# Performance work log

Measured on AMD Instinct MI355X. Metric: run time of the kernel, lower is better.

The kernel has to match this reference:

```python
import jax, jax.numpy as jnp
import numpy as np

N = 100000
E = 1600000
IN_CH, HID_CH, OUT_CH = 128, 64, 32


def setup_inputs() -> dict:
    key = jax.random.key(0)
    ks = jax.random.split(key, 6)
    x = jax.random.normal(ks[0], (N, IN_CH), dtype=jnp.float32)
    ei = jax.random.randint(ks[1], (2, E), 0, N, dtype=jnp.int64)
    W1 = jax.random.normal(ks[2], (IN_CH, HID_CH), dtype=jnp.float32) * 0.05
    b1 = jax.random.normal(ks[3], (HID_CH,), dtype=jnp.float32) * 0.05
    W2 = jax.random.normal(ks[4], (HID_CH, OUT_CH), dtype=jnp.float32) * 0.05
    b2 = jax.random.normal(ks[5], (OUT_CH,), dtype=jnp.float32) * 0.05
    return {"x": x, "ei": ei, "W1": W1, "b1": b1, "W2": W2, "b2": b2}


def gcn_layer(x, sa, da, n):
    # degree with self-loops already appended in sa/da
    deg = jax.ops.segment_sum(jnp.ones((sa.shape[0],), x.dtype), da, num_segments=n)
    prod = deg[sa] * deg[da]
    norm = jnp.where(prod > 0, jax.lax.rsqrt(prod), 0.0)  # (deg_s*deg_d)^-0.5, inf->0
    msg = x[sa] * norm[:, None]            # [E+N, C] gather + scale
    return jax.ops.segment_sum(msg, da, num_segments=n)  # scatter_add


def reference(x, ei, W1, b1, W2, b2):
    n = x.shape[0]
    loop = jnp.arange(n, dtype=ei.dtype)
    sa = jnp.concatenate([ei[0], loop])
    da = jnp.concatenate([ei[1], loop])
    h = gcn_layer(x @ W1 + b1, sa, da, n)
    h = jax.nn.relu(h)
    # dropout: eval mode (training=False) -> identity
    return gcn_layer(h @ W2 + b2, sa, da, n)
```

## Files before the change

### kernel.cpp

```cpp
#include <hip/hip_runtime.h>

#define NN 100000
#define NE 1600000
#define IN_CH 128
#define HID_CH 64
#define OUT_CH 32
#define NB2 98
#define CHUNKA 8192
#define NBLKA ((NE + CHUNKA - 1) / CHUNKA)
#define NBLK_GEMM ((NN + 63) / 64)

typedef unsigned short ushort_t;
typedef _Float16 half2_t __attribute__((ext_vector_type(2)));
typedef float f32x2 __attribute__((ext_vector_type(2)));

__device__ inline ushort_t f2bf(float f) {
    union { float f; unsigned u; } v; v.f = f;
    unsigned r = v.u + 0x7fff + ((v.u >> 16) & 1);
    return (ushort_t)(r >> 16);
}
__device__ inline float blo(unsigned u) {
    union { unsigned x; float f; } v; v.x = u << 16; return v.f;
}
__device__ inline float bhi(unsigned u) {
    union { unsigned x; float f; } v; v.x = u & 0xffff0000u; return v.f;
}
__device__ inline unsigned pkh(float a, float b) {
    union { half2_t h; unsigned u; } v;
    v.h[0] = (_Float16)a; v.h[1] = (_Float16)b;
    return v.u;
}
__device__ inline half2_t u2h(unsigned u) {
    union { unsigned u; half2_t h; } v; v.u = u; return v.h;
}
__device__ inline float fdot2(unsigned a, unsigned b, float c) {
#if __has_builtin(__builtin_amdgcn_fdot2)
    return __builtin_amdgcn_fdot2(u2h(a), u2h(b), c, false);
#else
    half2_t ha = u2h(a), hb = u2h(b);
    return c + (float)ha[0] * (float)hb[0] + (float)ha[1] * (float)hb[1];
#endif
}
__device__ inline f32x2 pk_add(f32x2 a, f32x2 b) {
    f32x2 r;
    asm("v_pk_add_f32 %0, %1, %2" : "=v"(r) : "v"(a), "v"(b));
    return r;
}

__global__ __launch_bounds__(256) void k_bhist(const int* __restrict__ da,
                                               int* __restrict__ bcnt,
                                               int* __restrict__ bhall) {
    __shared__ int hist[4][NB2];
    int t = threadIdx.x, w = t >> 6;
    for (int i = t; i < 4 * NB2; i += 256) ((int*)hist)[i] = 0;
    __syncthreads();
    int base = blockIdx.x * CHUNKA;
    for (int i = 0; i < CHUNKA; i += 256) {
        int e = base + i + t;
        if (e < NE) atomicAdd(&hist[w][da[e] >> 10], 1);
    }
    __syncthreads();
    if (t < NB2) {
        int c = hist[0][t] + hist[1][t] + hist[2][t] + hist[3][t];
        bhall[blockIdx.x * NB2 + t] = c;
        if (c) atomicAdd(&bcnt[t], c);
    }
}

__global__ __launch_bounds__(128) void k_bscan(const int* __restrict__ bcnt,
                                               int* __restrict__ bbase,
                                               int* __restrict__ bcur,
                                               int* __restrict__ rowptr) {
    __shared__ int lds[128];
    int t = threadIdx.x;
    int v = (t < NB2) ? bcnt[t] : 0;
    lds[t] = v;
    __syncthreads();
    for (int off = 1; off < 128; off <<= 1) {
        int x = (t >= off) ? lds[t - off] : 0;
        __syncthreads();
        lds[t] += x;
        __syncthreads();
    }
    int excl = lds[t] - v;
    if (t < NB2) { bbase[t] = excl; bcur[t] = excl; }
    if (t == 0) { bbase[NB2] = NE; rowptr[NN] = NE; }
}

__global__ __launch_bounds__(256) void k_bfill(const int* __restrict__ sa,
                                               const int* __restrict__ da,
                                               const int* __restrict__ bhall,
                                               int* __restrict__ bcur,
                                               unsigned* __restrict__ ebuf) {
    __shared__ int lcur[NB2];
    int t = threadIdx.x;
    if (t < NB2) {
        int c = bhall[blockIdx.x * NB2 + t];
        lcur[t] = c ? atomicAdd(&bcur[t], c) : 0;
    }
    __syncthreads();
    int base = blockIdx.x * CHUNKA;
    for (int i = 0; i < CHUNKA; i += 256) {
        int e = base + i + t;
        if (e < NE) {
            int d = da[e];
            int p = atomicAdd(&lcur[d >> 10], 1);
            ebuf[p] = ((unsigned)sa[e] << 10) | (unsigned)(d & 1023);
        }
    }
}

__global__ __launch_bounds__(1024) void k_bfine(const unsigned* __restrict__ ebuf,
                                                const int* __restrict__ bbase,
                                                int* __restrict__ rowptr,
                                                float* __restrict__ rs,
                                                int* __restrict__ col) {
    __shared__ int cnt[1024];
    __shared__ int cur[1024];
    __shared__ int scn[1024];
    int b = blockIdx.x, t = threadIdx.x;
    int nb = NN - b * 1024; if (nb > 1024) nb = 1024;
    int beg = bbase[b], end = bbase[b + 1];
    cnt[t] = 0;
    __syncthreads();
    for (int i = beg + t; i < end; i += 1024) atomicAdd(&cnt[ebuf[i] & 1023], 1);
    __syncthreads();
    int v = cnt[t];
    scn[t] = v;
    __syncthreads();
    for (int off = 1; off < 1024; off <<= 1) {
        int x = (t >= off) ? scn[t - off] : 0;
        __syncthreads();
        scn[t] += x;
        __syncthreads();
    }
    int excl = scn[t] - v;
    if (t < nb) {
        rowptr[b * 1024 + t] = beg + excl;
        rs[b * 1024 + t] = rsqrtf((float)(v + 1));
        cur[t] = beg + excl;
    }
    __syncthreads();
    for (int i = beg + t; i < end; i += 1024) {
        unsigned p = ebuf[i];
        int pos = atomicAdd(&cur[p & 1023], 1);
        col[pos] = (int)(p >> 10);
    }
}

#define SWZU1(n, k2) ((n) * 64 + ((k2) ^ ((((n) & 7)) << 2)))
#define SWZ2(n, k) ((n) * 64 + ((k) ^ ((((n) & 7)) << 2)))

__global__ __launch_bounds__(256, 4) void k_gemm1(
    const float* __restrict__ x, const float* __restrict__ W1,
    const float* __restrict__ b1, const float* __restrict__ rs,
    ushort_t* __restrict__ xsb) {
    __shared__ unsigned xth[64 * 64];
    __shared__ unsigned w1h[64 * 64];
    int t = threadIdx.x;
    int base = blockIdx.x * 64;

#pragma unroll
    for (int i = 0; i < 8; ++i) {
        int flat = i * 1024 + t * 4;
        int node = flat >> 7, k0 = flat & 127;
        int gn = base + node;
        float4 v = make_float4(0.f, 0.f, 0.f, 0.f);
        if (gn < NN) v = *(const float4*)(x + (size_t)gn * IN_CH + k0);
        uint2 pk;
        pk.x = pkh(v.x, v.y);
        pk.y = pkh(v.z, v.w);
        *(uint2*)&xth[SWZU1(node, k0 >> 1)] = pk;
    }
#pragma unroll
    for (int i = 0; i < 16; ++i) {
        int idx = i * 256 + t;
        int k2 = idx >> 6, c = idx & 63;
        float f0 = W1[(2 * k2) * 64 + c];
        float f1 = W1[(2 * k2 + 1) * 64 + c];
        w1h[idx] = pkh(f0, f1);
    }
    __syncthreads();

    int tn = t & 15, tc = t >> 4;
    int c0 = tc * 4;
    float acc[4][4];
#pragma unroll
    for (int a = 0; a < 4; ++a)
#pragma unroll
        for (int b = 0; b < 4; ++b) acc[a][b] = 0.f;

    for (int k2 = 0; k2 < 64; k2 += 2) {
        uint2 xu[4];
#pragma unroll
        for (int jn = 0; jn < 4; ++jn)
            xu[jn] = *(uint2*)&xth[SWZU1(tn + jn * 16, k2)];
        uint4 w0 = *(uint4*)&w1h[(k2 + 0) * 64 + c0];
        uint4 w1 = *(uint4*)&w1h[(k2 + 1) * 64 + c0];
        unsigned wq0[4] = {w0.x, w0.y, w0.z, w0.w};
        unsigned wq1[4] = {w1.x, w1.y, w1.z, w1.w};
#pragma unroll
        for (int jn = 0; jn < 4; ++jn)
#pragma unroll
            for (int jc = 0; jc < 4; ++jc) {
                acc[jn][jc] = fdot2(xu[jn].x, wq0[jc], acc[jn][jc]);
                acc[jn][jc] = fdot2(xu[jn].y, wq1[jc], acc[jn][jc]);
            }
    }

    float4 bb = *(const float4*)&b1[c0];
#pragma unroll
    for (int jn = 0; jn < 4; ++jn) {
        int gn = base + tn + jn * 16;
        if (gn < NN) {
            float r = rs[gn];
            uint2 pk;
            pk.x = (unsigned)f2bf((acc[jn][0] + bb.x) * r) |
                   ((unsigned)f2bf((acc[jn][1] + bb.y) * r) << 16);
            pk.y = (unsigned)f2bf((acc[jn][2] + bb.z) * r) |
                   ((unsigned)f2bf((acc[jn][3] + bb.w) * r) << 16);
            *(uint2*)&xsb[(size_t)gn * HID_CH + c0] = pk;
        }
    }
}

#define ADD8PK(v) do { \
    f32x2 w0_, w1_, w2_, w3_; \
    w0_.x = blo((v).x); w0_.y = bhi((v).x); p0 = pk_add(p0, w0_); \
    w1_.x = blo((v).y); w1_.y = bhi((v).y); p1 = pk_add(p1, w1_); \
    w2_.x = blo((v).z); w2_.y = bhi((v).z); p2 = pk_add(p2, w2_); \
    w3_.x = blo((v).w); w3_.y = bhi((v).w); p3 = pk_add(p3, w3_); } while (0)

__global__ __launch_bounds__(256) void k_agg1(
    const int* __restrict__ rowptr, const int* __restrict__ col,
    const ushort_t* __restrict__ xsb, const float* __restrict__ rs,
    ushort_t* __restrict__ hb) {
    int gid = blockIdx.x * blockDim.x + threadIdx.x;
    int n = gid >> 6;
    if (n >= NN) return;
    int lane = threadIdx.x & 63;
    int g = lane >> 3;
    unsigned c0 = (unsigned)(lane & 7) * 8;
    int beg = rowptr[n], end = rowptr[n + 1];

    f32x2 p0 = {0.f, 0.f}, p1 = {0.f, 0.f}, p2 = {0.f, 0.f}, p3 = {0.f, 0.f};
    if (g == 0) {
        uint4 sv = *(const uint4*)&xsb[(unsigned)n * 64u + c0];
        ADD8PK(sv);
    }

    int i = beg;
    for (; i + 16 <= end; i += 16) {
        int s0 = col[i + g];
        int s1 = col[i + 8 + g];
        uint4 v0 = *(const uint4*)&xsb[(unsigned)s0 * 64u + c0];
        uint4 v1 = *(const uint4*)&xsb[(unsigned)s1 * 64u + c0];
        ADD8PK(v0);
        ADD8PK(v1);
    }
    if (i + 8 <= end) {
        int s0 = col[i + g];
        uint4 v0 = *(const uint4*)&xsb[(unsigned)s0 * 64u + c0];
        ADD8PK(v0);
        i += 8;
    }
    int r = end - i;
    if (g < r) {
        int s0 = col[i + g];
        uint4 v0 = *(const uint4*)&xsb[(unsigned)s0 * 64u + c0];
        ADD8PK(v0);
    }

    float a0 = p0.x, a1 = p0.y, a2 = p1.x, a3 = p1.y;
    float a4 = p2.x, a5 = p2.y, a6 = p3.x, a7 = p3.y;
#pragma unroll
    for (int m = 8; m <= 32; m <<= 1) {
        a0 += __shfl_xor(a0, m); a1 += __shfl_xor(a1, m);
        a2 += __shfl_xor(a2, m); a3 += __shfl_xor(a3, m);
        a4 += __shfl_xor(a4, m); a5 += __shfl_xor(a5, m);
        a6 += __shfl_xor(a6, m); a7 += __shfl_xor(a7, m);
    }

    if (g == 0) {
        float rn = rs[n];
        uint4 pk;
        pk.x = (unsigned)f2bf(fmaxf(a0 * rn, 0.f)) |
               ((unsigned)f2bf(fmaxf(a1 * rn, 0.f)) << 16);
        pk.y = (unsigned)f2bf(fmaxf(a2 * rn, 0.f)) |
               ((unsigned)f2bf(fmaxf(a3 * rn, 0.f)) << 16);
        pk.z = (unsigned)f2bf(fmaxf(a4 * rn, 0.f)) |
               ((unsigned)f2bf(fmaxf(a5 * rn, 0.f)) << 16);
        pk.w = (unsigned)f2bf(fmaxf(a6 * rn, 0.f)) |
               ((unsigned)f2bf(fmaxf(a7 * rn, 0.f)) << 16);
        *(uint4*)&hb[(unsigned)n * 64u + c0] = pk;
    }
}

__global__ __launch_bounds__(256) void k_gemm2(
    const ushort_t* __restrict__ hb, const float* __restrict__ W2,
    const float* __restrict__ b2, const float* __restrict__ rs,
    ushort_t* __restrict__ ysb) {
    __shared__ float ht[64 * 64];
    __shared__ float w2s[64 * 32];
    int t = threadIdx.x;
    int base = blockIdx.x * 64;

#pragma unroll
    for (int i = 0; i < 8; ++i) {
        int uidx = i * 256 + t;
        int node = uidx >> 5, k2 = uidx & 31;
        int gn = base + node;
        unsigned u = 0;
        if (gn < NN) u = *(const unsigned*)&hb[(size_t)gn * HID_CH + k2 * 2];
        float2 f; f.x = blo(u); f.y = bhi(u);
        *(float2*)&ht[SWZ2(node, k2 * 2)] = f;
    }
#pragma unroll
    for (int i = 0; i < 2; ++i) {
        int flat = i * 1024 + t * 4;
        *(float4*)&w2s[flat] = *(const float4*)(W2 + flat);
    }
    __syncthreads();

    int tn = t & 15, tc = t >> 4;
    int c0 = tc * 2;
    float acc[4][2];
#pragma unroll
    for (int a = 0; a < 4; ++a) { acc[a][0] = 0.f; acc[a][1] = 0.f; }

    for (int k0 = 0; k0 < 64; k0 += 4) {
        float xq[4][4], wq[4][2];
#pragma unroll
        for (int j = 0; j < 4; ++j)
            *(float2*)&wq[j][0] = *(float2*)&w2s[(k0 + j) * 32 + c0];
#pragma unroll
        for (int jn = 0; jn < 4; ++jn)
            *(float4*)&xq[jn][0] = *(float4*)&ht[SWZ2(tn + jn * 16, k0)];
#pragma unroll
        for (int jn = 0; jn < 4; ++jn)
#pragma unroll
            for (int j = 0; j < 4; ++j) {
                acc[jn][0] = fmaf(xq[jn][j], wq[j][0], acc[jn][0]);
                acc[jn][1] = fmaf(xq[jn][j], wq[j][1], acc[jn][1]);
            }
    }

    float2 bb = *(const float2*)&b2[c0];
#pragma unroll
    for (int jn = 0; jn < 4; ++jn) {
        int gn = base + tn + jn * 16;
        if (gn < NN) {
            float r = rs[gn];
            unsigned pk = (unsigned)f2bf((acc[jn][0] + bb.x) * r) |
                          ((unsigned)f2bf((acc[jn][1] + bb.y) * r) << 16);
            *(unsigned*)&ysb[(size_t)gn * OUT_CH + c0] = pk;
        }
    }
}

__global__ __launch_bounds__(256) void k_agg2(
    const int* __restrict__ rowptr, const int* __restrict__ col,
    const ushort_t* __restrict__ ysb, const float* __restrict__ rs,
    float* __restrict__ out) {
    int gid = blockIdx.x * blockDim.x + threadIdx.x;
    int n = gid >> 6;
    if (n >= NN) return;
    int lane = threadIdx.x & 63;
    int g = lane >> 2;
    unsigned c0 = (unsigned)(lane & 3) * 8;
    int beg = rowptr[n], end = rowptr[n + 1];

    f32x2 p0 = {0.f, 0.f}, p1 = {0.f, 0.f}, p2 = {0.f, 0.f}, p3 = {0.f, 0.f};
    if (g == 0) {
        uint4 sv = *(const uint4*)&ysb[(unsigned)n * 32u + c0];
        ADD8PK(sv);
    }

    int i = beg;
    for (; i + 16 <= end; i += 16) {
        int s0 = col[i + g];
        uint4 v0 = *(const uint4*)&ysb[(unsigned)s0 * 32u + c0];
        ADD8PK(v0);
    }
    int r = end - i;
    if (g < r) {
        int s0 = col[i + g];
        uint4 v0 = *(const uint4*)&ysb[(unsigned)s0 * 32u + c0];
        ADD8PK(v0);
    }

    float a0 = p0.x, a1 = p0.y, a2 = p1.x, a3 = p1.y;
    float a4 = p2.x, a5 = p2.y, a6 = p3.x, a7 = p3.y;
#pragma unroll
    for (int m = 4; m <= 32; m <<= 1) {
        a0 += __shfl_xor(a0, m); a1 += __shfl_xor(a1, m);
        a2 += __shfl_xor(a2, m); a3 += __shfl_xor(a3, m);
        a4 += __shfl_xor(a4, m); a5 += __shfl_xor(a5, m);
        a6 += __shfl_xor(a6, m); a7 += __shfl_xor(a7, m);
    }

    if (g == 0) {
        float rn = rs[n];
        float4 o0, o1;
        o0.x = a0 * rn; o0.y = a1 * rn; o0.z = a2 * rn; o0.w = a3 * rn;
        o1.x = a4 * rn; o1.y = a5 * rn; o1.z = a6 * rn; o1.w = a7 * rn;
        *(float4*)&out[(size_t)n * OUT_CH + c0] = o0;
        *(float4*)&out[(size_t)n * OUT_CH + c0 + 4] = o1;
    }
}

extern "C" void kernel_launch(void* const* d_in, const int* in_sizes, int n_in,
                              void* d_out, int out_size, void* d_ws, size_t ws_size,
                              hipStream_t stream) {
    const float* x  = (const float*)d_in[0];
    const int*   ei = (const int*)d_in[1];
    const float* W1 = (const float*)d_in[2];
    const float* b1 = (const float*)d_in[3];
    const float* W2 = (const float*)d_in[4];
    const float* b2 = (const float*)d_in[5];
    const int* sa = ei;
    const int* da = ei + NE;

    char* ws = (char*)d_ws;
    size_t off = 0;
    auto alloc = [&](size_t bytes) {
        void* p = ws + off;
        off += (bytes + 255) & ~(size_t)255;
        return p;
    };
    int*      bcnt   = (int*)alloc((size_t)NB2 * 4);
    int*      bbase  = (int*)alloc((size_t)(NB2 + 1) * 4);
    int*      bcur   = (int*)alloc((size_t)NB2 * 4);
    int*      bhall  = (int*)alloc((size_t)NBLKA * NB2 * 4);
    int*      rowptr = (int*)alloc((size_t)(NN + 1) * 4);
    float*    rs     = (float*)alloc((size_t)NN * 4);
    unsigned* ebuf   = (unsigned*)alloc((size_t)NE * 4);
    int*      col    = (int*)alloc((size_t)NE * 4);
    ushort_t* xsb    = (ushort_t*)alloc((size_t)NN * HID_CH * 2);
    ushort_t* hb     = (ushort_t*)alloc((size_t)NN * HID_CH * 2);
    ushort_t* ysb    = (ushort_t*)alloc((size_t)NN * OUT_CH * 2);
    float*    outp   = (float*)d_out;

    const int B = 256;
    hipMemsetAsync(bcnt, 0, (size_t)NB2 * 4, stream);
    k_bhist<<<NBLKA, 256, 0, stream>>>(da, bcnt, bhall);
    k_bscan<<<1, 128, 0, stream>>>(bcnt, bbase, bcur, rowptr);
    k_bfill<<<NBLKA, 256, 0, stream>>>(sa, da, bhall, bcur, ebuf);
    k_bfine<<<NB2, 1024, 0, stream>>>(ebuf, bbase, rowptr, rs, col);

    k_gemm1<<<NBLK_GEMM, 256, 0, stream>>>(x, W1, b1, rs, xsb);
    k_agg1<<<(NN * 64 + B - 1) / B, B, 0, stream>>>(rowptr, col, xsb, rs, hb);
    k_gemm2<<<NBLK_GEMM, 256, 0, stream>>>(hb, W2, b2, rs, ysb);
    k_agg2<<<(NN * 64 + B - 1) / B, B, 0, stream>>>(rowptr, col, ysb, rs, outp);
}
```

Before: 218.2 us.

## Split fine bucket pass and overlap column scatter with first GEMM

The fine bucketing kernel is split so that counting, scanning, rowptr and rs are computed in one kernel. The column scatter now runs as the first NB2 blocks of a combined kernel whose remaining blocks do the first GEMM, so the two can run concurrently on the GPU. The scatter blocks use 256 threads instead of 1024 and each walks a bucket of about 16K edges, so those blocks may become the long tail. The combined kernel also needs an extra 4KB of shared memory per block, which may lower GEMM occupancy.

```diff
diff --git a/kernel.cpp b/kernel.cpp
--- a/kernel.cpp
+++ b/kernel.cpp
@@ -110,13 +110,11 @@
     }
 }
 
-__global__ __launch_bounds__(1024) void k_bfine(const unsigned* __restrict__ ebuf,
-                                                const int* __restrict__ bbase,
-                                                int* __restrict__ rowptr,
-                                                float* __restrict__ rs,
-                                                int* __restrict__ col) {
+__global__ __launch_bounds__(1024) void k_bcount(const unsigned* __restrict__ ebuf,
+                                                 const int* __restrict__ bbase,
+                                                 int* __restrict__ rowptr,
+                                                 float* __restrict__ rs) {
     __shared__ int cnt[1024];
-    __shared__ int cur[1024];
     __shared__ int scn[1024];
     int b = blockIdx.x, t = threadIdx.x;
     int nb = NN - b * 1024; if (nb > 1024) nb = 1024;
@@ -138,28 +136,41 @@
     if (t < nb) {
         rowptr[b * 1024 + t] = beg + excl;
         rs[b * 1024 + t] = rsqrtf((float)(v + 1));
-        cur[t] = beg + excl;
-    }
-    __syncthreads();
-    for (int i = beg + t; i < end; i += 1024) {
-        unsigned p = ebuf[i];
-        int pos = atomicAdd(&cur[p & 1023], 1);
-        col[pos] = (int)(p >> 10);
     }
 }
 
 #define SWZU1(n, k2) ((n) * 64 + ((k2) ^ ((((n) & 7)) << 2)))
 #define SWZ2(n, k) ((n) * 64 + ((k) ^ ((((n) & 7)) << 2)))
 
-__global__ __launch_bounds__(256, 4) void k_gemm1(
+__global__ __launch_bounds__(256, 4) void k_scatter_gemm1(
+    const unsigned* __restrict__ ebuf, const int* __restrict__ rowptr,
+    const int* __restrict__ bbase, int* __restrict__ col,
     const float* __restrict__ x, const float* __restrict__ W1,
     const float* __restrict__ b1, const float* __restrict__ rs,
     ushort_t* __restrict__ xsb) {
     __shared__ unsigned xth[64 * 64];
     __shared__ unsigned w1h[64 * 64];
+    __shared__ int cur[1024];
     int t = threadIdx.x;
-    int base = blockIdx.x * 64;
-
+
+    if (blockIdx.x < NB2) {
+        int b = blockIdx.x;
+#pragma unroll
+        for (int j = 0; j < 4; ++j) {
+            int n = b * 1024 + j * 256 + t;
+            cur[j * 256 + t] = (n < NN) ? rowptr[n] : 0;
+        }
+        int beg = bbase[b], end = bbase[b + 1];
+        __syncthreads();
+        for (int i = beg + t; i < end; i += 256) {
+            unsigned w = ebuf[i];
+            int pos = atomicAdd(&cur[w & 1023], 1);
+            col[pos] = (int)(w >> 10);
+        }
+        return;
+    }
+
+    int base = (blockIdx.x - NB2) * 64;
 #pragma unroll
     for (int i = 0; i < 8; ++i) {
         int flat = i * 1024 + t * 4;
@@ -446,9 +457,9 @@
     k_bhist<<<NBLKA, 256, 0, stream>>>(da, bcnt, bhall);
     k_bscan<<<1, 128, 0, stream>>>(bcnt, bbase, bcur, rowptr);
     k_bfill<<<NBLKA, 256, 0, stream>>>(sa, da, bhall, bcur, ebuf);
-    k_bfine<<<NB2, 1024, 0, stream>>>(ebuf, bbase, rowptr, rs, col);
-
-    k_gemm1<<<NBLK_GEMM, 256, 0, stream>>>(x, W1, b1, rs, xsb);
+    k_bcount<<<NB2, 1024, 0, stream>>>(ebuf, bbase, rowptr, rs);
+    k_scatter_gemm1<<<NB2 + NBLK_GEMM, 256, 0, stream>>>(ebuf, rowptr, bbase, col,
+                                                         x, W1, b1, rs, xsb);
     k_agg1<<<(NN * 64 + B - 1) / B, B, 0, stream>>>(rowptr, col, xsb, rs, hb);
     k_gemm2<<<NBLK_GEMM, 256, 0, stream>>>(hb, W2, b2, rs, ysb);
     k_agg2<<<(NN * 64 + B - 1) / B, B, 0, stream>>>(rowptr, col, ysb, rs, outp);
```

Result: faster. 210.1 us, median of 2 (-3.7%).
